# Performance work log

Measured on AMD Instinct MI355X. Metric: run time of the kernel, lower is better.

## Reference

```python
import jax, jax.numpy as jnp
import numpy as np

SX = 512; SY = 512; C = 3; NK = 10; R = 10
DT = 0.2; DD = 5; SIGMA = 0.65; THETA_A = 1.0; NPOW = 2


def setup_inputs() -> dict:
    rng = np.random.RandomState(0)
    r = rng.uniform(0.3, 1.0, NK).astype(np.float32)
    m = rng.uniform(0.05, 0.5, NK).astype(np.float32)
    s = rng.uniform(0.01, 0.18, NK).astype(np.float32)
    h = rng.uniform(0.2, 1.0, NK).astype(np.float32)
    a = rng.uniform(0.0, 1.0, (NK, 3)).astype(np.float32)
    w = rng.uniform(0.01, 0.5, (NK, 3)).astype(np.float32)
    b = rng.uniform(0.0, 1.0, (NK, 3)).astype(np.float32)
    # compute_kernel(): radial distance grid, ring sigmoid * sum-of-bumps ker_f, normalized
    mid = SX // 2
    x = np.linspace(-mid, mid, 2 * mid, dtype=np.float32)
    X, Y = np.meshgrid(x, x, indexing='ij')
    dist = np.sqrt(X ** 2 + Y ** 2)
    D = dist[:, :, None] / ((R + 15.0) * r)                      # (SX, SY, NK)
    ring = 1.0 / (1.0 + np.exp((D - 1.0) * 10.0))                # sigmoid(-(D-1)*10)
    bumps = (b * np.exp(-((D[..., None] - a) ** 2) / w)).sum(-1)  # ker_f(D, a, w, b)
    K = (ring * bumps).astype(np.float32)
    nK_ker = K / K.sum(axis=(0, 1), keepdims=True)               # (SX, SY, NK)
    # kernel -> source channel, and kernel -> target channel one-hot (c1 as matrix)
    c0 = np.array([0, 0, 0, 1, 1, 1, 2, 2, 2, 0], dtype=np.int32)
    tgt = np.array([0, 1, 2, 0, 1, 2, 0, 1, 2, 0], dtype=np.int32)
    c1_mat = np.zeros((NK, C), dtype=np.int32)
    c1_mat[np.arange(NK), tgt] = 1
    key = jax.random.key(0)
    A = jax.random.uniform(key, (SX, SY, C), dtype=jnp.float32)  # scale_init_state = 1
    return {"A": A, "nK_ker": jnp.asarray(nK_ker), "m": jnp.asarray(m),
            "s": jnp.asarray(s), "h": jnp.asarray(h),
            "c0": jnp.asarray(c0), "c1_mat": jnp.asarray(c1_mat)}


def _sobel(A):
    """A: (SX, SY, Cc) -> (SX, SY, 2, Cc), circular (toroidal) boundary."""
    def grad_ax(ax):
        sm_ax = 1 - ax
        sm = jnp.roll(A, 1, sm_ax) + 2.0 * A + jnp.roll(A, -1, sm_ax)  # [1,2,1] smoothing
        return (jnp.roll(sm, -1, ax) - jnp.roll(sm, 1, ax)) / 8.0       # central diff
    return jnp.stack([grad_ax(0), grad_ax(1)], axis=2)


def _flowlenia_step(A, nK_ker, m, s, h, c0, c1_mat):
    # FFT Lenia convolution
    fA = jnp.fft.fft2(A, axes=(0, 1))                              # (SX, SY, C) complex
    fK = jnp.fft.fft2(jnp.fft.fftshift(nK_ker, axes=(0, 1)), axes=(0, 1))
    U = jnp.real(jnp.fft.ifft2(fK * fA[:, :, c0], axes=(0, 1)))    # (SX, SY, NK)
    # growth * h, then gather-sum kernels into target channels (c1)
    U = (2.0 * jnp.exp(-((U - m) ** 2) / (2.0 * s ** 2)) - 1.0) * h
    U = jnp.einsum('xyk,kc->xyc', U, c1_mat.astype(U.dtype))       # (SX, SY, C)
    # flow field
    nabla_U = _sobel(U)                                            # (SX, SY, 2, C)
    nabla_A = _sobel(A.sum(-1, keepdims=True))                     # (SX, SY, 2, 1)
    alpha = jnp.clip((A[:, :, None, :] / THETA_A) ** NPOW, 0.0, 1.0)
    F = nabla_U * (1.0 - alpha) - nabla_A * alpha                  # (SX, SY, 2, C)
    # reintegration tracking (mass-conserving advection over (2*DD+1)^2 shifts)
    xs = jnp.arange(SX, dtype=A.dtype)
    ys = jnp.arange(SY, dtype=A.dtype)
    X, Y = jnp.meshgrid(xs, ys, indexing='ij')
    pos = jnp.stack([X, Y], axis=-1) + 0.5                         # (SX, SY, 2) cell centers
    ma = DD - SIGMA                                                # max flow magnitude
    mu = pos[..., None] + DT * jnp.clip(F, -ma, ma)                # (SX, SY, 2, C)
    shifts = jnp.array([(dx, dy) for dx in range(-DD, DD + 1)
                        for dy in range(-DD, DD + 1)], dtype=jnp.int32)
    clip_hi = min(1.0, 2.0 * SIGMA)
    inv_norm = 1.0 / (4.0 * SIGMA ** 2)

    def body(acc, sh):
        dx, dy = sh[0], sh[1]
        rA = jnp.roll(jnp.roll(A, dx, 0), dy, 1)
        rmu = jnp.roll(jnp.roll(mu, dx, 0), dy, 1)
        sz = 0.5 - jnp.abs(pos[..., None] - rmu) + SIGMA
        area = jnp.prod(jnp.clip(sz, 0.0, clip_hi), axis=2) * inv_norm  # (SX, SY, C)
        return acc + rA * area, None

    nA, _ = jax.lax.scan(body, jnp.zeros_like(A), shifts)
    return nA


def reference(A, nK_ker, m, s, h, c0, c1_mat):
    return _flowlenia_step(A, nK_ker, m, s, h, c0, c1_mat)
```

## Files before the change

### kernel.cpp

```cpp
#include <hip/hip_runtime.h>
#include <math.h>

#define NF 512
#define NF2 (NF * NF)
#define RPB 4
#define ROWLEN 580
#define PI_F 3.14159265358979323846f

#define LPAD(q) ((q) + ((q) >> 3))

__device__ inline float2 cadd(float2 a, float2 b) { return make_float2(a.x + b.x, a.y + b.y); }
__device__ inline float2 csub(float2 a, float2 b) { return make_float2(a.x - b.x, a.y - b.y); }
__device__ inline float2 cmul(float2 a, float2 b) {
    return make_float2(a.x * b.x - a.y * b.y, a.x * b.y + a.y * b.x);
}

__device__ inline void fft8(float2 x[8], float dsign) {
    const float s = 0.70710678118654752440f;
    float2 a0 = cadd(x[0], x[4]), a1 = cadd(x[1], x[5]);
    float2 a2 = cadd(x[2], x[6]), a3 = cadd(x[3], x[7]);
    float2 b0 = csub(x[0], x[4]), b1 = csub(x[1], x[5]);
    float2 b2 = csub(x[2], x[6]), b3 = csub(x[3], x[7]);
    b1 = cmul(b1, make_float2(s, dsign * s));
    b2 = make_float2(-dsign * b2.y, dsign * b2.x);
    b3 = cmul(b3, make_float2(-s, dsign * s));
    float2 c0 = cadd(a0, a2), c1 = cadd(a1, a3);
    float2 c2 = csub(a0, a2), c3 = csub(a1, a3);
    c3 = make_float2(-dsign * c3.y, dsign * c3.x);
    float2 d0 = cadd(b0, b2), d1 = cadd(b1, b3);
    float2 d2 = csub(b0, b2), d3 = csub(b1, b3);
    d3 = make_float2(-dsign * d3.y, dsign * d3.x);
    x[0] = cadd(c0, c1); x[4] = csub(c0, c1);
    x[2] = cadd(c2, c3); x[6] = csub(c2, c3);
    x[1] = cadd(d0, d1); x[5] = csub(d0, d1);
    x[3] = cadd(d2, d3); x[7] = csub(d2, d3);
}

__device__ inline void twiddle8(float2 x[8], float2 wb) {
    float2 tw = wb;
    x[1] = cmul(x[1], tw); tw = cmul(tw, wb);
    x[2] = cmul(x[2], tw); tw = cmul(tw, wb);
    x[3] = cmul(x[3], tw); tw = cmul(tw, wb);
    x[4] = cmul(x[4], tw); tw = cmul(tw, wb);
    x[5] = cmul(x[5], tw); tw = cmul(tw, wb);
    x[6] = cmul(x[6], tw); tw = cmul(tw, wb);
    x[7] = cmul(x[7], tw);
}

__device__ inline void fft512_regs(float2 x[8], int b, float2* bufA, float2* bufB,
                                   const float2* Wt, float dsign) {
    fft8(x, dsign);
    float2 wb0 = make_float2(Wt[b].x, dsign * Wt[b].y);
    twiddle8(x, wb0);
#pragma unroll
    for (int p = 0; p < 8; ++p) bufA[9 * b + p] = x[p];
    __syncthreads();
#pragma unroll
    for (int j = 0; j < 8; ++j) x[j] = bufA[LPAD(b + 64 * j)];
    fft8(x, dsign);
    int u = b >> 3, v = b & 7;
    float2 wb1 = make_float2(Wt[b & ~7].x, dsign * Wt[b & ~7].y);
    twiddle8(x, wb1);
    int base = u * 64 + v;
#pragma unroll
    for (int p = 0; p < 8; ++p) bufB[LPAD(base + 8 * p)] = x[p];
    __syncthreads();
#pragma unroll
    for (int j = 0; j < 8; ++j) x[j] = bufB[LPAD(b + 64 * j)];
    fft8(x, dsign);
}

#define FFT_PRE                                                    \
    __shared__ float2 SHA[RPB][ROWLEN];                            \
    __shared__ float2 SHB[RPB][ROWLEN];                            \
    __shared__ float2 Wt[512];                                     \
    int tid = threadIdx.x;                                         \
    int rr_ = tid >> 6, bb_ = tid & 63;                            \
    {                                                              \
        float sn, cs;                                              \
        sincosf((PI_F / 256.0f) * (float)tid, &sn, &cs);           \
        Wt[tid] = make_float2(cs, sn);                             \
        sincosf((PI_F / 256.0f) * (float)(tid + 256), &sn, &cs);   \
        Wt[tid + 256] = make_float2(cs, sn);                       \
    }

__device__ inline float2 unpack_field(const float2* __restrict__ Z, int plane, int slot,
                                      int ky, int kx) {
    const float2* P = Z + (size_t)plane * NF2;
    float2 zr = P[(ky << 9) + kx];
    float2 zm = P[(((NF - ky) & (NF - 1)) << 9) + ((NF - kx) & (NF - 1))];
    if (slot == 0)
        return make_float2(0.5f * (zr.x + zm.x), 0.5f * (zr.y - zm.y));
    else
        return make_float2(0.5f * (zr.y + zm.y), 0.5f * (zm.x - zr.x));
}

__global__ __launch_bounds__(256) void k_fwd_p1(const float* __restrict__ A,
                                                const float* __restrict__ K,
                                                float2* __restrict__ Z) {
    FFT_PRE
    int pl = blockIdx.y;
    const float* bre; int sre, cre;
    const float* bim; int sim, cim;
    switch (pl) {
        case 0: bre = A; sre = 3; cre = 0; bim = A; sim = 3; cim = 1; break;
        case 1: bre = A; sre = 3; cre = 2; bim = K; sim = 10; cim = 0; break;
        case 2: bre = K; sre = 10; cre = 1; bim = K; sim = 10; cim = 2; break;
        case 3: bre = K; sre = 10; cre = 3; bim = K; sim = 10; cim = 4; break;
        case 4: bre = K; sre = 10; cre = 5; bim = K; sim = 10; cim = 6; break;
        case 5: bre = K; sre = 10; cre = 7; bim = K; sim = 10; cim = 8; break;
        default: bre = K; sre = 10; cre = 9; bim = nullptr; sim = 0; cim = 0; break;
    }
    int x0 = blockIdx.x * RPB;
    int row = x0 + rr_;
    float2 x[8];
#pragma unroll
    for (int j = 0; j < 8; ++j) {
        int idx = (row << 9) + bb_ + 64 * j;
        float vr = bre[idx * sre + cre];
        float vi = bim ? bim[idx * sim + cim] : 0.0f;
        x[j] = make_float2(vr, vi);
    }
    __syncthreads();
    fft512_regs(x, bb_, &SHA[rr_][0], &SHB[rr_][0], Wt, -1.0f);
#pragma unroll
    for (int p2 = 0; p2 < 8; ++p2) SHA[rr_][LPAD(64 * p2 + bb_)] = x[p2];
    __syncthreads();
    for (int i = tid; i < RPB * NF; i += 256) {
        int r2 = i & (RPB - 1), ky = i >> 2;
        Z[(size_t)((pl << 9) + ky) * NF + x0 + r2] = SHA[r2][LPAD(ky)];
    }
}

__global__ __launch_bounds__(256) void k_fft_rows(float2* __restrict__ data, float dsign) {
    FFT_PRE
    int R0 = blockIdx.x * RPB;
    size_t rowbase = (size_t)(R0 + rr_) * NF;
    float2 x[8];
#pragma unroll
    for (int j = 0; j < 8; ++j) x[j] = data[rowbase + bb_ + 64 * j];
    __syncthreads();
    fft512_regs(x, bb_, &SHA[rr_][0], &SHB[rr_][0], Wt, dsign);
#pragma unroll
    for (int p2 = 0; p2 < 8; ++p2) SHA[rr_][LPAD(64 * p2 + bb_)] = x[p2];
    __syncthreads();
    for (int i = tid; i < RPB * NF; i += 256) {
        int r2 = i >> 9, xx = i & (NF - 1);
        data[(size_t)(R0 + r2) * NF + xx] = SHA[r2][LPAD(xx)];
    }
}

__global__ __launch_bounds__(256) void k_mulinv_p1(const float2* __restrict__ Z,
                                                   const int* __restrict__ c0,
                                                   float2* __restrict__ tmp) {
    FFT_PRE
    int jp = blockIdx.y;
    int k1 = 2 * jp, k2 = 2 * jp + 1;
    int pK1 = (k1 == 0) ? 1 : 2 + ((k1 - 1) >> 1);
    int sK1 = (k1 == 0) ? 1 : ((k1 - 1) & 1);
    int pK2 = 2 + ((k2 - 1) >> 1);
    int sK2 = (k2 - 1) & 1;
    int cA1 = c0[k1], cA2 = c0[k2];
    int pA1 = cA1 >> 1, sA1 = cA1 & 1;
    int pA2 = cA2 >> 1, sA2 = cA2 & 1;
    bool sameA = (cA1 == cA2);

    int ky0 = blockIdx.x * RPB;
    int ky = ky0 + rr_;
    float2 x[8];
#pragma unroll
    for (int jj = 0; jj < 8; ++jj) {
        int kx = bb_ + 64 * jj;
        float2 fk1 = unpack_field(Z, pK1, sK1, ky, kx);
        float2 fk2 = unpack_field(Z, pK2, sK2, ky, kx);
        float2 fa1 = unpack_field(Z, pA1, sA1, ky, kx);
        float2 fa2 = sameA ? fa1 : unpack_field(Z, pA2, sA2, ky, kx);
        float t1x = fk1.x * fa1.x - fk1.y * fa1.y;
        float t1y = fk1.x * fa1.y + fk1.y * fa1.x;
        float t2x = fk2.x * fa2.x - fk2.y * fa2.y;
        float t2y = fk2.x * fa2.y + fk2.y * fa2.x;
        float sgn = ((kx + ky) & 1) ? -1.0f : 1.0f;
        x[jj] = make_float2((t1x - t2y) * sgn, (t1y + t2x) * sgn);
    }
    __syncthreads();
    fft512_regs(x, bb_, &SHA[rr_][0], &SHB[rr_][0], Wt, +1.0f);
#pragma unroll
    for (int p2 = 0; p2 < 8; ++p2) SHA[rr_][LPAD(64 * p2 + bb_)] = x[p2];
    __syncthreads();
    for (int i = tid; i < RPB * NF; i += 256) {
        int r2 = i & (RPB - 1), xx = i >> 2;
        tmp[(size_t)(jp * NF + xx) * NF + ky0 + r2] = SHA[r2][LPAD(xx)];
    }
}

__global__ __launch_bounds__(256) void k_inv_p2g(const float2* __restrict__ tmp,
                                                 const float* __restrict__ mm,
                                                 const float* __restrict__ ss,
                                                 const float* __restrict__ hh,
                                                 float* __restrict__ G) {
    FFT_PRE
    int jp = blockIdx.y;
    int k1 = 2 * jp, k2 = 2 * jp + 1;
    int x0 = blockIdx.x * RPB;
    int row = x0 + rr_;
    size_t base = (size_t)(jp * NF + row) * NF;
    float2 x[8];
#pragma unroll
    for (int j2 = 0; j2 < 8; ++j2) x[j2] = tmp[base + bb_ + 64 * j2];
    __syncthreads();
    fft512_regs(x, bb_, &SHA[rr_][0], &SHB[rr_][0], Wt, +1.0f);
    float m1 = mm[k1], s1 = ss[k1], h1 = hh[k1];
    float m2 = mm[k2], s2 = ss[k2], h2 = hh[k2];
    float i2s1 = 1.0f / (2.0f * s1 * s1);
    float i2s2 = 1.0f / (2.0f * s2 * s2);
    const float scale = 1.0f / ((float)NF * (float)NF);
#pragma unroll
    for (int p2 = 0; p2 < 8; ++p2) {
        int y = 64 * p2 + bb_;
        float u1 = x[p2].x * scale, u2 = x[p2].y * scale;
        float d1 = u1 - m1, d2 = u2 - m2;
        size_t o = (size_t)row * NF + y;
        G[(size_t)k1 * NF2 + o] = (2.0f * expf(-d1 * d1 * i2s1) - 1.0f) * h1;
        G[(size_t)k2 * NF2 + o] = (2.0f * expf(-d2 * d2 * i2s2) - 1.0f) * h2;
    }
}

__global__ __launch_bounds__(256) void k_combine(const float* __restrict__ G,
                                                 const int* __restrict__ c1,
                                                 const float* __restrict__ A,
                                                 float* __restrict__ Up,
                                                 float* __restrict__ As) {
    int id = blockIdx.x * 256 + threadIdx.x;
    float a0 = 0.f, a1 = 0.f, a2 = 0.f;
#pragma unroll
    for (int k = 0; k < 10; ++k) {
        float g = G[k * NF2 + id];
        a0 += g * (float)c1[k * 3 + 0];
        a1 += g * (float)c1[k * 3 + 1];
        a2 += g * (float)c1[k * 3 + 2];
    }
    Up[id] = a0;
    Up[NF2 + id] = a1;
    Up[2 * NF2 + id] = a2;
    As[id] = A[id * 3 + 0] + A[id * 3 + 1] + A[id * 3 + 2];
}

__global__ __launch_bounds__(256) void k_flow(const float* __restrict__ Up,
                                              const float* __restrict__ As,
                                              const float* __restrict__ A,
                                              float* __restrict__ mu) {
    int id = blockIdx.x * 256 + threadIdx.x;
    int x = id >> 9, y = id & (NF - 1);
    int xm = (x - 1) & (NF - 1), xp = (x + 1) & (NF - 1);
    int ym = (y - 1) & (NF - 1), yp = (y + 1) & (NF - 1);

    auto grad = [&](const float* f, float& gx, float& gy) {
        float fmm = f[xm * NF + ym], fm0 = f[xm * NF + y], fmp = f[xm * NF + yp];
        float f0m = f[x * NF + ym], f0p = f[x * NF + yp];
        float fpm = f[xp * NF + ym], fp0 = f[xp * NF + y], fpp = f[xp * NF + yp];
        gx = (fpm + 2.0f * fp0 + fpp - fmm - 2.0f * fm0 - fmp) * 0.125f;
        gy = (fmp + 2.0f * f0p + fpp - fmm - 2.0f * f0m - fpm) * 0.125f;
    };

    float gax, gay;
    grad(As, gax, gay);
    float px = (float)x + 0.5f, py = (float)y + 0.5f;
#pragma unroll
    for (int c = 0; c < 3; ++c) {
        float gux, guy;
        grad(Up + c * NF2, gux, guy);
        float a = A[id * 3 + c];
        float al = fminf(a * a, 1.0f);
        float Fx = gux * (1.0f - al) - gax * al;
        float Fy = guy * (1.0f - al) - gay * al;
        Fx = fminf(fmaxf(Fx, -4.35f), 4.35f);
        Fy = fminf(fmaxf(Fy, -4.35f), 4.35f);
        mu[c * NF2 + id] = px + 0.2f * Fx;
        mu[(3 + c) * NF2 + id] = py + 0.2f * Fy;
    }
}

__global__ __launch_bounds__(256) void k_reint(const float* __restrict__ A,
                                               const float* __restrict__ mu,
                                               float* __restrict__ out) {
    __shared__ float sA[3][36 * 36];
    __shared__ float sM[6][36 * 36];
    int tid = threadIdx.x;
    int x0 = blockIdx.x * 32, y0 = blockIdx.y * 32;
    for (int i = tid; i < 36 * 36; i += 256) {
        int lx = i / 36, ly = i - lx * 36;
        int xg = (x0 - 2 + lx) & (NF - 1);
        int yg = (y0 - 2 + ly) & (NF - 1);
        int gid = xg * NF + yg;
        sA[0][i] = A[gid * 3 + 0];
        sA[1][i] = A[gid * 3 + 1];
        sA[2][i] = A[gid * 3 + 2];
#pragma unroll
        for (int p = 0; p < 6; ++p) sM[p][i] = mu[p * NF2 + gid];
    }
    __syncthreads();

    const float INV_NORM = (float)(1.0 / (4.0 * 0.65 * 0.65));
    int cy = tid & 31, cx0 = tid >> 5;
    for (int sidx = 0; sidx < 4; ++sidx) {
        int cx = cx0 + 8 * sidx;
        int x = x0 + cx, y = y0 + cy;
        float px = (float)x + 0.5f, py = (float)y + 0.5f;
        float acc0 = 0.f, acc1 = 0.f, acc2 = 0.f;
#pragma unroll
        for (int dx = 0; dx < 5; ++dx)
#pragma unroll
            for (int dy = 0; dy < 5; ++dy) {
                int li = (cx + dx) * 36 + (cy + dy);
#pragma unroll
                for (int c = 0; c < 3; ++c) {
                    float mux = sM[c][li], muy = sM[3 + c][li];
                    float szx = 0.5f - fabsf(px - mux) + 0.65f;
                    float szy = 0.5f - fabsf(py - muy) + 0.65f;
                    szx = fminf(fmaxf(szx, 0.0f), 1.0f);
                    szy = fminf(fmaxf(szy, 0.0f), 1.0f);
                    float area = szx * szy * INV_NORM;
                    float v = sA[c][li] * area;
                    if (c == 0) acc0 += v;
                    else if (c == 1) acc1 += v;
                    else acc2 += v;
                }
            }
        int gid = x * NF + y;
        out[gid * 3 + 0] = acc0;
        out[gid * 3 + 1] = acc1;
        out[gid * 3 + 2] = acc2;
    }
}

extern "C" void kernel_launch(void* const* d_in, const int* in_sizes, int n_in,
                              void* d_out, int out_size, void* d_ws, size_t ws_size,
                              hipStream_t stream) {
    (void)in_sizes; (void)n_in; (void)out_size; (void)ws_size;
    const float* A  = (const float*)d_in[0];
    const float* nK = (const float*)d_in[1];
    const float* m  = (const float*)d_in[2];
    const float* s  = (const float*)d_in[3];
    const float* h  = (const float*)d_in[4];
    const int*   c0 = (const int*)d_in[5];
    const int*   c1 = (const int*)d_in[6];
    float* out = (float*)d_out;

    char* ws = (char*)d_ws;
    float2* Z   = (float2*)ws;
    float2* tmp = (float2*)(ws + 14680064);
    float*  G   = (float*)ws;
    float*  Up  = (float*)(ws + 10485760);
    float*  As  = (float*)(ws + 13631488);
    float*  mu  = (float*)(ws + 14680064);

    dim3 blk(256);
    k_fwd_p1<<<dim3(NF / RPB, 7), blk, 0, stream>>>(A, nK, Z);
    k_fft_rows<<<dim3(7 * NF / RPB), blk, 0, stream>>>(Z, -1.0f);
    k_mulinv_p1<<<dim3(NF / RPB, 5), blk, 0, stream>>>(Z, c0, tmp);
    k_inv_p2g<<<dim3(NF / RPB, 5),   blk, 0, stream>>>(tmp, m, s, h, G);
    k_combine<<<dim3(NF2 / 256), blk, 0, stream>>>(G, c1, A, Up, As);
    k_flow<<<dim3(NF2 / 256),    blk, 0, stream>>>(Up, As, A, mu);
    k_reint<<<dim3(16, 16),      blk, 0, stream>>>(A, mu, out);
}
```

Before: 142.5 us.

## Fuse combine, flow and reintegration kernels into one tiled tail kernel

Replaces the three final kernels (channel combine, Sobel flow, advection reintegration) with a single kernel working on 32x32 tiles. Each tile loads G and A with a 3-cell halo into shared memory, computes the combined update field and the flow-derived mu for a 2-cell halo in shared memory, and then does the reintegration. This removes the global round-trips of the Up, As and mu arrays and two kernel launches. In exchange the halo regions are computed redundantly, shared memory use per block rises, and only 256 blocks run, which may lower occupancy.

```diff
diff --git a/kernel.cpp b/kernel.cpp
--- a/kernel.cpp
+++ b/kernel.cpp
@@ -225,78 +225,76 @@
     }
 }
 
-__global__ __launch_bounds__(256) void k_combine(const float* __restrict__ G,
-                                                 const int* __restrict__ c1,
-                                                 const float* __restrict__ A,
-                                                 float* __restrict__ Up,
-                                                 float* __restrict__ As) {
-    int id = blockIdx.x * 256 + threadIdx.x;
-    float a0 = 0.f, a1 = 0.f, a2 = 0.f;
+#define HT 38
+#define HT2 (HT * HT)
+#define CT 36
+#define CT2 (CT * CT)
+__global__ __launch_bounds__(256) void k_tail(const float* __restrict__ G,
+                                              const int* __restrict__ c1,
+                                              const float* __restrict__ A,
+                                              float* __restrict__ out) {
+    __shared__ float sUp[3][HT2];
+    __shared__ float sAs[HT2];
+    __shared__ float sA[3][HT2];
+    __shared__ float sM[6][CT2];
+    int tid = threadIdx.x;
+    int X0 = blockIdx.x * 32, Y0 = blockIdx.y * 32;
+
+    float w0[10], w1[10], w2[10];
 #pragma unroll
     for (int k = 0; k < 10; ++k) {
-        float g = G[k * NF2 + id];
-        a0 += g * (float)c1[k * 3 + 0];
-        a1 += g * (float)c1[k * 3 + 1];
-        a2 += g * (float)c1[k * 3 + 2];
-    }
-    Up[id] = a0;
-    Up[NF2 + id] = a1;
-    Up[2 * NF2 + id] = a2;
-    As[id] = A[id * 3 + 0] + A[id * 3 + 1] + A[id * 3 + 2];
-}
-
-__global__ __launch_bounds__(256) void k_flow(const float* __restrict__ Up,
-                                              const float* __restrict__ As,
-                                              const float* __restrict__ A,
-                                              float* __restrict__ mu) {
-    int id = blockIdx.x * 256 + threadIdx.x;
-    int x = id >> 9, y = id & (NF - 1);
-    int xm = (x - 1) & (NF - 1), xp = (x + 1) & (NF - 1);
-    int ym = (y - 1) & (NF - 1), yp = (y + 1) & (NF - 1);
-
-    auto grad = [&](const float* f, float& gx, float& gy) {
-        float fmm = f[xm * NF + ym], fm0 = f[xm * NF + y], fmp = f[xm * NF + yp];
-        float f0m = f[x * NF + ym], f0p = f[x * NF + yp];
-        float fpm = f[xp * NF + ym], fp0 = f[xp * NF + y], fpp = f[xp * NF + yp];
-        gx = (fpm + 2.0f * fp0 + fpp - fmm - 2.0f * fm0 - fmp) * 0.125f;
-        gy = (fmp + 2.0f * f0p + fpp - fmm - 2.0f * f0m - fpm) * 0.125f;
-    };
-
-    float gax, gay;
-    grad(As, gax, gay);
-    float px = (float)x + 0.5f, py = (float)y + 0.5f;
-#pragma unroll
-    for (int c = 0; c < 3; ++c) {
-        float gux, guy;
-        grad(Up + c * NF2, gux, guy);
-        float a = A[id * 3 + c];
-        float al = fminf(a * a, 1.0f);
-        float Fx = gux * (1.0f - al) - gax * al;
-        float Fy = guy * (1.0f - al) - gay * al;
-        Fx = fminf(fmaxf(Fx, -4.35f), 4.35f);
-        Fy = fminf(fmaxf(Fy, -4.35f), 4.35f);
-        mu[c * NF2 + id] = px + 0.2f * Fx;
-        mu[(3 + c) * NF2 + id] = py + 0.2f * Fy;
-    }
-}
-
-__global__ __launch_bounds__(256) void k_reint(const float* __restrict__ A,
-                                               const float* __restrict__ mu,
-                                               float* __restrict__ out) {
-    __shared__ float sA[3][36 * 36];
-    __shared__ float sM[6][36 * 36];
-    int tid = threadIdx.x;
-    int x0 = blockIdx.x * 32, y0 = blockIdx.y * 32;
-    for (int i = tid; i < 36 * 36; i += 256) {
-        int lx = i / 36, ly = i - lx * 36;
-        int xg = (x0 - 2 + lx) & (NF - 1);
-        int yg = (y0 - 2 + ly) & (NF - 1);
+        w0[k] = (float)c1[k * 3 + 0];
+        w1[k] = (float)c1[k * 3 + 1];
+        w2[k] = (float)c1[k * 3 + 2];
+    }
+
+    for (int i = tid; i < HT2; i += 256) {
+        int lx = i / HT, ly = i - lx * HT;
+        int xg = (X0 - 3 + lx) & (NF - 1);
+        int yg = (Y0 - 3 + ly) & (NF - 1);
         int gid = xg * NF + yg;
-        sA[0][i] = A[gid * 3 + 0];
-        sA[1][i] = A[gid * 3 + 1];
-        sA[2][i] = A[gid * 3 + 2];
-#pragma unroll
-        for (int p = 0; p < 6; ++p) sM[p][i] = mu[p * NF2 + gid];
+        float a0 = 0.f, a1 = 0.f, a2 = 0.f;
+#pragma unroll
+        for (int k = 0; k < 10; ++k) {
+            float g = G[(size_t)k * NF2 + gid];
+            a0 += g * w0[k]; a1 += g * w1[k]; a2 += g * w2[k];
+        }
+        sUp[0][i] = a0; sUp[1][i] = a1; sUp[2][i] = a2;
+        float A0 = A[gid * 3 + 0], A1 = A[gid * 3 + 1], A2 = A[gid * 3 + 2];
+        sA[0][i] = A0; sA[1][i] = A1; sA[2][i] = A2;
+        sAs[i] = A0 + A1 + A2;
+    }
+    __syncthreads();
+
+    for (int i = tid; i < CT2; i += 256) {
+        int lx = i / CT, ly = i - lx * CT;
+        int ci = (lx + 1) * HT + (ly + 1);
+        int xg = (X0 - 2 + lx) & (NF - 1);
+        int yg = (Y0 - 2 + ly) & (NF - 1);
+
+        auto grad38 = [&](const float* f, float& gx, float& gy) {
+            float fmm = f[ci - HT - 1], fm0 = f[ci - HT], fmp = f[ci - HT + 1];
+            float f0m = f[ci - 1], f0p = f[ci + 1];
+            float fpm = f[ci + HT - 1], fp0 = f[ci + HT], fpp = f[ci + HT + 1];
+            gx = (fpm + 2.0f * fp0 + fpp - fmm - 2.0f * fm0 - fmp) * 0.125f;
+            gy = (fmp + 2.0f * f0p + fpp - fmm - 2.0f * f0m - fpm) * 0.125f;
+        };
+        float gax, gay;
+        grad38(sAs, gax, gay);
+        float px = (float)xg + 0.5f, py = (float)yg + 0.5f;
+#pragma unroll
+        for (int c = 0; c < 3; ++c) {
+            float gux, guy;
+            grad38(sUp[c], gux, guy);
+            float a = sA[c][ci];
+            float al = fminf(a * a, 1.0f);
+            float Fx = gux * (1.0f - al) - gax * al;
+            float Fy = guy * (1.0f - al) - gay * al;
+            Fx = fminf(fmaxf(Fx, -4.35f), 4.35f);
+            Fy = fminf(fmaxf(Fy, -4.35f), 4.35f);
+            sM[c][i] = px + 0.2f * Fx;
+            sM[3 + c][i] = py + 0.2f * Fy;
+        }
     }
     __syncthreads();
 
@@ -304,23 +302,24 @@
     int cy = tid & 31, cx0 = tid >> 5;
     for (int sidx = 0; sidx < 4; ++sidx) {
         int cx = cx0 + 8 * sidx;
-        int x = x0 + cx, y = y0 + cy;
+        int x = X0 + cx, y = Y0 + cy;
         float px = (float)x + 0.5f, py = (float)y + 0.5f;
         float acc0 = 0.f, acc1 = 0.f, acc2 = 0.f;
 #pragma unroll
         for (int dx = 0; dx < 5; ++dx)
 #pragma unroll
             for (int dy = 0; dy < 5; ++dy) {
-                int li = (cx + dx) * 36 + (cy + dy);
+                int li36 = (cx + dx) * CT + (cy + dy);
+                int li38 = (cx + dx + 1) * HT + (cy + dy + 1);
 #pragma unroll
                 for (int c = 0; c < 3; ++c) {
-                    float mux = sM[c][li], muy = sM[3 + c][li];
+                    float mux = sM[c][li36], muy = sM[3 + c][li36];
                     float szx = 0.5f - fabsf(px - mux) + 0.65f;
                     float szy = 0.5f - fabsf(py - muy) + 0.65f;
                     szx = fminf(fmaxf(szx, 0.0f), 1.0f);
                     szy = fminf(fmaxf(szy, 0.0f), 1.0f);
                     float area = szx * szy * INV_NORM;
-                    float v = sA[c][li] * area;
+                    float v = sA[c][li38] * area;
                     if (c == 0) acc0 += v;
                     else if (c == 1) acc1 += v;
                     else acc2 += v;
@@ -350,16 +349,11 @@
     float2* Z   = (float2*)ws;
     float2* tmp = (float2*)(ws + 14680064);
     float*  G   = (float*)ws;
-    float*  Up  = (float*)(ws + 10485760);
-    float*  As  = (float*)(ws + 13631488);
-    float*  mu  = (float*)(ws + 14680064);
 
     dim3 blk(256);
     k_fwd_p1<<<dim3(NF / RPB, 7), blk, 0, stream>>>(A, nK, Z);
     k_fft_rows<<<dim3(7 * NF / RPB), blk, 0, stream>>>(Z, -1.0f);
     k_mulinv_p1<<<dim3(NF / RPB, 5), blk, 0, stream>>>(Z, c0, tmp);
     k_inv_p2g<<<dim3(NF / RPB, 5),   blk, 0, stream>>>(tmp, m, s, h, G);
-    k_combine<<<dim3(NF2 / 256), blk, 0, stream>>>(G, c1, A, Up, As);
-    k_flow<<<dim3(NF2 / 256),    blk, 0, stream>>>(Up, As, A, mu);
-    k_reint<<<dim3(16, 16),      blk, 0, stream>>>(A, mu, out);
-}
+    k_tail<<<dim3(16, 16), blk, 0, stream>>>(G, c1, A, out);
+}
```

Result: faster. 135.0 us (-5.3%).
